# Kernel tuning notes

Hardware: AMD Instinct MI355X
Metric: run time of the kernel (lower is better)

## Reference

```python
import jax, jax.numpy as jnp
import numpy as np

D = 512        # feat_dim
H_ENC = 8      # motion_encoder heads
H_SA = 4       # semantic-aware attention heads
BS, L, N = 8, 512, 4096
LN_EPS = 1e-5


def _layernorm(x, g, b):
    m = jnp.mean(x, axis=-1, keepdims=True)
    v = jnp.var(x, axis=-1, keepdims=True)
    return (x - m) * jax.lax.rsqrt(v + LN_EPS) * g + b


def _linear(x, w, b):
    # torch nn.Linear convention: w [out, in]
    return x @ w.T + b


def setup_inputs() -> dict:
    key = jax.random.key(0)
    ks = jax.random.split(key, 24)
    s = 0.02
    inp = {
        "motion": jax.random.normal(ks[0], (BS, L, D), jnp.float32),
        "scene_xyz": jax.random.normal(ks[1], (BS, N, 3), jnp.float32),
        "scene_feats": jax.random.normal(ks[2], (BS, N, D), jnp.float32),
        "spatial_prior": jax.random.normal(ks[3], (BS, L, N), jnp.float32),
        # motion_encoder (pre-norm MHA + pre-norm MLP, both residual)
        "enc_ln1_g": jnp.ones((D,), jnp.float32),
        "enc_ln1_b": jnp.zeros((D,), jnp.float32),
        "enc_qkv_w": jax.random.normal(ks[4], (3 * D, D), jnp.float32) * s,
        "enc_qkv_b": jnp.zeros((3 * D,), jnp.float32),
        "enc_out_w": jax.random.normal(ks[5], (D, D), jnp.float32) * s,
        "enc_out_b": jnp.zeros((D,), jnp.float32),
        "enc_ln2_g": jnp.ones((D,), jnp.float32),
        "enc_ln2_b": jnp.zeros((D,), jnp.float32),
        "enc_ff1_w": jax.random.normal(ks[6], (D, D), jnp.float32) * s,
        "enc_ff1_b": jnp.zeros((D,), jnp.float32),
        "enc_ff2_w": jax.random.normal(ks[7], (D, D), jnp.float32) * s,
        "enc_ff2_b": jnp.zeros((D,), jnp.float32),
        # SemanticAwareAttention
        "sa_q_w": jax.random.normal(ks[8], (D, D), jnp.float32) * s,
        "sa_q_b": jnp.zeros((D,), jnp.float32),
        "sa_kv_w": jax.random.normal(ks[9], (2 * D, D), jnp.float32) * s,
        "sa_kv_b": jnp.zeros((2 * D,), jnp.float32),
        "sa_out_w": jax.random.normal(ks[10], (D, D), jnp.float32) * s,
        "sa_out_b": jnp.zeros((D,), jnp.float32),
        # final concat-MLP: in 2D -> 4D -> D  (Mlp(2D, D, expansion=4))
        "mlp_fc1_w": jax.random.normal(ks[11], (4 * D, 2 * D), jnp.float32) * s,
        "mlp_fc1_b": jnp.zeros((4 * D,), jnp.float32),
        "mlp_fc2_w": jax.random.normal(ks[12], (D, 4 * D), jnp.float32) * s,
        "mlp_fc2_b": jnp.zeros((D,), jnp.float32),
    }
    return inp


def _forward(motion, scene_xyz, scene_feats, spatial_prior,
             enc_ln1_g, enc_ln1_b, enc_qkv_w, enc_qkv_b, enc_out_w, enc_out_b,
             enc_ln2_g, enc_ln2_b, enc_ff1_w, enc_ff1_b, enc_ff2_w, enc_ff2_b,
             sa_q_w, sa_q_b, sa_kv_w, sa_kv_b, sa_out_w, sa_out_b,
             mlp_fc1_w, mlp_fc1_b, mlp_fc2_w, mlp_fc2_b):
    bs, slen, _ = motion.shape
    n = scene_feats.shape[1]
    dh_enc = D // H_ENC
    dh_sa = D // H_SA

    # ---- motion encoder: pre-norm MHA + residual ----
    h = _layernorm(motion, enc_ln1_g, enc_ln1_b)
    qkv = _linear(h, enc_qkv_w, enc_qkv_b)                      # [bs, L, 3D]
    q, k, v = jnp.split(qkv, 3, axis=-1)
    q = q.reshape(bs, slen, H_ENC, dh_enc)
    k = k.reshape(bs, slen, H_ENC, dh_enc)
    v = v.reshape(bs, slen, H_ENC, dh_enc)
    att = jnp.einsum("bqhd,bkhd->bhqk", q, k) * (dh_enc ** -0.5)
    att = jax.nn.softmax(att, axis=-1)
    o = jnp.einsum("bhqk,bkhd->bqhd", att, v).reshape(bs, slen, D)
    x = motion + _linear(o, enc_out_w, enc_out_b)

    # ---- pre-norm MLP + residual ----
    h2 = _layernorm(x, enc_ln2_g, enc_ln2_b)
    ff = _linear(jax.nn.gelu(_linear(h2, enc_ff1_w, enc_ff1_b), approximate=False),
                 enc_ff2_w, enc_ff2_b)
    motion_sca = x + ff

    # ---- SemanticAwareAttention ----
    q = _linear(motion_sca, sa_q_w, sa_q_b) * (D ** -0.5)       # scale by feat_dim (faithful)
    kv = _linear(scene_feats, sa_kv_w, sa_kv_b)
    k, v = jnp.split(kv, 2, axis=-1)
    # faithful to torch: q.view(bs, H, L, d) splits heads from flattened (L, D)
    q = q.reshape(bs, H_SA, slen, dh_sa)
    k = k.reshape(bs, n, H_SA, dh_sa).transpose(0, 2, 1, 3)     # [bs, H, N, d]
    v = v.reshape(bs, n, H_SA, dh_sa).transpose(0, 2, 1, 3)
    att = jnp.einsum("bhqd,bhkd->bhqk", q, k) + spatial_prior[:, None, :, :]
    att = jax.nn.softmax(att, axis=-1)
    sm = jnp.einsum("bhqk,bhkd->bqhd", att, v).reshape(bs, slen, D)
    sm_feature = _linear(sm, sa_out_w, sa_out_b)

    # ---- concat + MLP ----
    cat = jnp.concatenate([motion_sca, sm_feature], axis=-1)    # [bs, L, 2D]
    out = _linear(jax.nn.gelu(_linear(cat, mlp_fc1_w, mlp_fc1_b), approximate=False),
                  mlp_fc2_w, mlp_fc2_b)
    return out


def reference(motion, scene_xyz, scene_feats, spatial_prior,
              enc_ln1_g, enc_ln1_b, enc_qkv_w, enc_qkv_b, enc_out_w, enc_out_b,
              enc_ln2_g, enc_ln2_b, enc_ff1_w, enc_ff1_b, enc_ff2_w, enc_ff2_b,
              sa_q_w, sa_q_b, sa_kv_w, sa_kv_b, sa_out_w, sa_out_b,
              mlp_fc1_w, mlp_fc1_b, mlp_fc2_w, mlp_fc2_b):
    return _forward(motion, scene_xyz, scene_feats, spatial_prior,
                    enc_ln1_g, enc_ln1_b, enc_qkv_w, enc_qkv_b, enc_out_w, enc_out_b,
                    enc_ln2_g, enc_ln2_b, enc_ff1_w, enc_ff1_b, enc_ff2_w, enc_ff2_b,
                    sa_q_w, sa_q_b, sa_kv_w, sa_kv_b, sa_out_w, sa_out_b,
                    mlp_fc1_w, mlp_fc1_b, mlp_fc2_w, mlp_fc2_b)
```

## Files before the change

kernel.cpp:

```cpp
#include <hip/hip_runtime.h>

typedef unsigned short bf16_t;
typedef __attribute__((ext_vector_type(8))) short bf16x8;
typedef __attribute__((ext_vector_type(4))) float f32x4;

__device__ __forceinline__ float bf2f(bf16_t u) {
  union { unsigned int i; float f; } v; v.i = ((unsigned int)u) << 16; return v.f;
}
__device__ __forceinline__ bf16_t f2bf(float f) {
  union { float f; unsigned int i; } v; v.f = f;
  unsigned int u = v.i;
  u += 0x7fffu + ((u >> 16) & 1u);
  return (bf16_t)(u >> 16);
}
__device__ __forceinline__ float gelu_exact(float x) {
  return 0.5f * x * (1.0f + erff(x * 0.7071067811865475f));
}

__global__ __launch_bounds__(256) void f2bf_kernel(const float4* __restrict__ s,
                                                   ushort4* __restrict__ d, int n4) {
  int i = blockIdx.x * 256 + threadIdx.x;
  if (i < n4) {
    float4 f = s[i];
    ushort4 u; u.x = f2bf(f.x); u.y = f2bf(f.y); u.z = f2bf(f.z); u.w = f2bf(f.w);
    d[i] = u;
  }
}

__global__ __launch_bounds__(256) void ln_kernel(const float* __restrict__ x,
                                                 const float* __restrict__ g,
                                                 const float* __restrict__ bta,
                                                 bf16_t* __restrict__ y) {
  const int w = threadIdx.x >> 6, lane = threadIdx.x & 63;
  const long row = (long)blockIdx.x * 4 + w;
  const long base = row * 512;
  const int c0 = lane << 2;
  float v[8];
  float4 f0 = *(const float4*)(x + base + c0);
  float4 f1 = *(const float4*)(x + base + 256 + c0);
  v[0]=f0.x; v[1]=f0.y; v[2]=f0.z; v[3]=f0.w;
  v[4]=f1.x; v[5]=f1.y; v[6]=f1.z; v[7]=f1.w;
  float s = 0.f;
#pragma unroll
  for (int c=0;c<8;++c) s += v[c];
#pragma unroll
  for (int o=32;o>0;o>>=1) s += __shfl_xor(s, o);
  const float mean = s * 0.001953125f;
  float ss = 0.f;
#pragma unroll
  for (int c=0;c<8;++c) { float d = v[c]-mean; ss += d*d; }
#pragma unroll
  for (int o=32;o>0;o>>=1) ss += __shfl_xor(ss, o);
  const float rstd = rsqrtf(ss * 0.001953125f + 1e-5f);
  ushort4 o0, o1;
  o0.x = f2bf((v[0]-mean)*rstd*g[c0+0] + bta[c0+0]);
  o0.y = f2bf((v[1]-mean)*rstd*g[c0+1] + bta[c0+1]);
  o0.z = f2bf((v[2]-mean)*rstd*g[c0+2] + bta[c0+2]);
  o0.w = f2bf((v[3]-mean)*rstd*g[c0+3] + bta[c0+3]);
  o1.x = f2bf((v[4]-mean)*rstd*g[256+c0+0] + bta[256+c0+0]);
  o1.y = f2bf((v[5]-mean)*rstd*g[256+c0+1] + bta[256+c0+1]);
  o1.z = f2bf((v[6]-mean)*rstd*g[256+c0+2] + bta[256+c0+2]);
  o1.w = f2bf((v[7]-mean)*rstd*g[256+c0+3] + bta[256+c0+3]);
  *(ushort4*)(y + base + c0) = o0;
  *(ushort4*)(y + base + 256 + c0) = o1;
}

struct MmaNT {
  const bf16_t* A; const bf16_t* W; const float* bias; const float* res; void* C;
  long lda, sAb, sAh;
  long ldw, sWb, sWh;
  long ldr, sRb, sRh;
  long ldc, sCb, sCh;
  int K, zdiv, cBf, act;
  float scale;
};

template <int MT>
__global__ __launch_bounds__(256) void mma_nt_kernel(MmaNT p) {
  constexpr int FM = MT / 32;
  __shared__ __align__(16) bf16_t smem[MT * 128];
  const int tid = threadIdx.x;
  const int wid = tid >> 6, lane = tid & 63;
  const int wm = wid & 1, wn = wid >> 1;
  const int quad = lane >> 4, l16 = lane & 15;
  const int z = blockIdx.z;
  const int zb = z / p.zdiv, zh = z % p.zdiv;

  const int nbx = gridDim.x;
  const int nwg = nbx * gridDim.y;
  const int flat = blockIdx.y * nbx + blockIdx.x;
  const int sw = (flat & 7) * (nwg >> 3) + (flat >> 3);
  const int bx = sw % nbx, by = sw / nbx;

  const long m0 = (long)by * MT;
  const long n0 = (long)bx * 128;
  const bf16_t* Ag = p.A + (long)zb * p.sAb + (long)zh * p.sAh +
                     (m0 + wm * (MT / 2) + l16) * p.lda;
  const bf16_t* Wg = p.W + (long)zb * p.sWb + (long)zh * p.sWh +
                     (n0 + wn * 64 + l16) * p.ldw;

  f32x4 zero4 = {0.f, 0.f, 0.f, 0.f};
  f32x4 acc[FM][4];
#pragma unroll
  for (int fm = 0; fm < FM; ++fm)
#pragma unroll
    for (int fn = 0; fn < 4; ++fn) acc[fm][fn] = zero4;

  bf16x8 af[FM], wf[4];
#pragma unroll
  for (int fm = 0; fm < FM; ++fm)
    af[fm] = *(const bf16x8*)(Ag + (long)(fm * 16) * p.lda + quad * 8);
#pragma unroll
  for (int fn = 0; fn < 4; ++fn)
    wf[fn] = *(const bf16x8*)(Wg + (long)(fn * 16) * p.ldw + quad * 8);

  for (int kc = 0; kc < p.K; kc += 32) {
    bf16x8 afn[FM], wfn[4];
    const int kn = kc + 32;
    if (kn < p.K) {
#pragma unroll
      for (int fm = 0; fm < FM; ++fm)
        afn[fm] = *(const bf16x8*)(Ag + (long)(fm * 16) * p.lda + kn + quad * 8);
#pragma unroll
      for (int fn = 0; fn < 4; ++fn)
        wfn[fn] = *(const bf16x8*)(Wg + (long)(fn * 16) * p.ldw + kn + quad * 8);
    }
#pragma unroll
    for (int fm = 0; fm < FM; ++fm)
#pragma unroll
      for (int fn = 0; fn < 4; ++fn)
        acc[fm][fn] = __builtin_amdgcn_mfma_f32_16x16x32_bf16(af[fm], wf[fn], acc[fm][fn], 0, 0, 0);
#pragma unroll
    for (int fm = 0; fm < FM; ++fm) af[fm] = afn[fm];
#pragma unroll
    for (int fn = 0; fn < 4; ++fn) wf[fn] = wfn[fn];
  }

  const long cOff = (long)zb * p.sCb + (long)zh * p.sCh;
  const long rOff = (long)zb * p.sRb + (long)zh * p.sRh;
  if (p.cBf) {
#pragma unroll
    for (int fm = 0; fm < FM; ++fm) {
#pragma unroll
      for (int fn = 0; fn < 4; ++fn) {
        const int lc = wn * 64 + fn * 16 + l16;
        const long col = n0 + lc;
        const float bv = p.bias ? p.bias[col] : 0.f;
#pragma unroll
        for (int r = 0; r < 4; ++r) {
          const int lr = wm * (MT / 2) + fm * 16 + quad * 4 + r;
          float t = acc[fm][fn][r] + bv;
          if (p.act) t = gelu_exact(t);
          t *= p.scale;
          if (p.res) t += p.res[rOff + (m0 + lr) * p.ldr + col];
          smem[lr * 128 + lc] = f2bf(t);
        }
      }
    }
    __syncthreads();
    bf16_t* Cg = (bf16_t*)p.C + cOff + m0 * p.ldc + n0;
#pragma unroll
    for (int i = 0; i < MT / 16; ++i) {
      const int flat2 = tid + i * 256;
      const int r = flat2 >> 4, c = (flat2 & 15) * 8;
      *(uint4*)(Cg + (long)r * p.ldc + c) = *(const uint4*)&smem[r * 128 + c];
    }
  } else {
#pragma unroll
    for (int fm = 0; fm < FM; ++fm) {
#pragma unroll
      for (int fn = 0; fn < 4; ++fn) {
        const long col = n0 + wn * 64 + fn * 16 + l16;
        const float bv = p.bias ? p.bias[col] : 0.f;
#pragma unroll
        for (int r = 0; r < 4; ++r) {
          const long row = m0 + wm * (MT / 2) + fm * 16 + quad * 4 + r;
          float t = acc[fm][fn][r] + bv;
          if (p.act) t = gelu_exact(t);
          t *= p.scale;
          if (p.res) t += p.res[rOff + row * p.ldr + col];
          ((float*)p.C)[cOff + row * p.ldc + col] = t;
        }
      }
    }
  }
}

struct TransP {
  const bf16_t* src; bf16_t* dst;
  long sSb, sSh, ld;
  int nh, N, D;
};

__global__ __launch_bounds__(256) void transpose_kernel(TransP p) {
  __shared__ bf16_t T[64][72];
  const int tid = threadIdx.x;
  const int z = blockIdx.z;
  const int zb = z / p.nh, zh = z % p.nh;
  const long n0 = (long)blockIdx.x * 64;
  const long d0 = (long)blockIdx.y * 64;
  const bf16_t* src = p.src + (long)zb * p.sSb + (long)zh * p.sSh;
  bf16_t* dst = p.dst + (long)z * p.D * p.N;
#pragma unroll
  for (int i = 0; i < 2; ++i) {
    int flat = tid + i * 256, r = flat >> 3, cg = flat & 7;
    uint4 v = *(const uint4*)(src + (n0 + r) * p.ld + d0 + cg * 8);
    *(uint4*)&T[r][cg * 8] = v;
  }
  __syncthreads();
#pragma unroll
  for (int i = 0; i < 2; ++i) {
    int flat = tid + i * 256, dr = flat >> 3, ncg = flat & 7;
    uint4 o;
    unsigned int* op = (unsigned int*)&o;
#pragma unroll
    for (int j = 0; j < 4; ++j)
      op[j] = (unsigned int)T[ncg * 8 + 2 * j][dr] | ((unsigned int)T[ncg * 8 + 2 * j + 1][dr] << 16);
    *(uint4*)(dst + (d0 + dr) * p.N + n0 + ncg * 8) = o;
  }
}

struct FlashP2 {
  const bf16_t* Q; const bf16_t* K; const bf16_t* VT; const float* prior;
  float* partO; float* partML;
  long ldq, sQb, sQh;
  long ldk, sKb, sKh;
  long sVz, sPb;
  int nh, N, segN;
  float scale;
};

template <int DH, int HASP>
__global__ __launch_bounds__(256) void flash3_kernel(FlashP2 p) {
  constexpr int KK = DH / 32;
  constexpr int NFO = DH / 16;
  constexpr int KPAD = DH + 8;
  __shared__ bf16_t smem[64 * KPAD + DH * 72];
  bf16_t* Kl = smem;
  bf16_t* Pl = smem;
  bf16_t* Vl = smem + 64 * KPAD;
  const int tid = threadIdx.x;
  const int w = tid >> 6, lane = tid & 63;
  const int quad = lane >> 4, l16 = lane & 15;
  const int z = blockIdx.z;
  const int zb = z / p.nh, zh = z % p.nh;
  const int qr0 = blockIdx.y * 64 + w * 16;
  const bf16_t* Q = p.Q + (long)zb * p.sQb + (long)zh * p.sQh + (long)qr0 * p.ldq;
  const bf16_t* K = p.K + (long)zb * p.sKb + (long)zh * p.sKh;
  const bf16_t* VT = p.VT + (long)z * p.sVz;

  bf16x8 qf[KK];
#pragma unroll
  for (int kk = 0; kk < KK; ++kk)
    qf[kk] = *(const bf16x8*)(Q + (long)l16 * p.ldq + kk * 32 + quad * 8);

  f32x4 zero4 = {0.f, 0.f, 0.f, 0.f};
  f32x4 O[NFO];
  float m_[4], l_[4];
#pragma unroll
  for (int f = 0; f < NFO; ++f) O[f] = zero4;
#pragma unroll
  for (int r = 0; r < 4; ++r) { m_[r] = -1e30f; l_[r] = 0.f; }

  const int k0 = blockIdx.x * p.segN;
  for (int kt = k0; kt < k0 + p.segN; kt += 64) {
    __syncthreads();
    constexpr int KTH = DH / 8;
#pragma unroll
    for (int i = 0; i < DH / 32; ++i) {
      int flat = tid + i * 256, r = flat / KTH, c = (flat % KTH) * 8;
      *(uint4*)&Kl[r * KPAD + c] = *(const uint4*)(K + (long)(kt + r) * p.ldk + c);
    }
#pragma unroll
    for (int i = 0; i < DH / 32; ++i) {
      int flat = tid + i * 256, r = flat >> 3, c = (flat & 7) * 8;
      *(uint4*)&Vl[r * 72 + c] = *(const uint4*)(VT + (long)r * p.N + kt + c);
    }
    float pr[4][4];
    if (HASP) {
      const float* PR = p.prior + (long)zb * p.sPb +
                        (long)(qr0 + quad * 4) * p.N + kt;
#pragma unroll
      for (int nf = 0; nf < 4; ++nf)
#pragma unroll
        for (int r = 0; r < 4; ++r)
          pr[nf][r] = PR[(long)r * p.N + nf * 16 + l16];
    }
    __syncthreads();
    f32x4 s[4];
#pragma unroll
    for (int nf = 0; nf < 4; ++nf) s[nf] = zero4;
#pragma unroll
    for (int nf = 0; nf < 4; ++nf)
#pragma unroll
      for (int kk = 0; kk < KK; ++kk) {
        bf16x8 kf = *(const bf16x8*)&Kl[(nf * 16 + l16) * KPAD + kk * 32 + quad * 8];
        s[nf] = __builtin_amdgcn_mfma_f32_16x16x32_bf16(qf[kk], kf, s[nf], 0, 0, 0);
      }
    float tm[4];
#pragma unroll
    for (int r = 0; r < 4; ++r) tm[r] = -1e30f;
#pragma unroll
    for (int nf = 0; nf < 4; ++nf)
#pragma unroll
      for (int r = 0; r < 4; ++r) {
        float t = s[nf][r] * p.scale;
        if (HASP) t += pr[nf][r];
        s[nf][r] = t;
        tm[r] = fmaxf(tm[r], t);
      }
#pragma unroll
    for (int off = 1; off < 16; off <<= 1)
#pragma unroll
      for (int r = 0; r < 4; ++r) tm[r] = fmaxf(tm[r], __shfl_xor(tm[r], off));
    float alpha[4], rs[4];
#pragma unroll
    for (int r = 0; r < 4; ++r) {
      float mn = fmaxf(m_[r], tm[r]);
      alpha[r] = __expf(m_[r] - mn);
      m_[r] = mn;
      rs[r] = 0.f;
    }
#pragma unroll
    for (int nf = 0; nf < 4; ++nf)
#pragma unroll
      for (int r = 0; r < 4; ++r) {
        float pv = __expf(s[nf][r] - m_[r]);
        s[nf][r] = pv;
        rs[r] += pv;
      }
#pragma unroll
    for (int off = 1; off < 16; off <<= 1)
#pragma unroll
      for (int r = 0; r < 4; ++r) rs[r] += __shfl_xor(rs[r], off);
#pragma unroll
    for (int r = 0; r < 4; ++r) l_[r] = l_[r] * alpha[r] + rs[r];
    __syncthreads();
#pragma unroll
    for (int nf = 0; nf < 4; ++nf)
#pragma unroll
      for (int r = 0; r < 4; ++r)
        Pl[(w * 16 + quad * 4 + r) * 72 + nf * 16 + l16] = f2bf(s[nf][r]);
#pragma unroll
    for (int f = 0; f < NFO; ++f)
#pragma unroll
      for (int r = 0; r < 4; ++r) O[f][r] *= alpha[r];
    bf16x8 pf[2];
#pragma unroll
    for (int kk2 = 0; kk2 < 2; ++kk2)
      pf[kk2] = *(const bf16x8*)&Pl[(w * 16 + l16) * 72 + kk2 * 32 + quad * 8];
#pragma unroll
    for (int f = 0; f < NFO; ++f)
#pragma unroll
      for (int kk2 = 0; kk2 < 2; ++kk2) {
        bf16x8 vf = *(const bf16x8*)&Vl[(f * 16 + l16) * 72 + kk2 * 32 + quad * 8];
        O[f] = __builtin_amdgcn_mfma_f32_16x16x32_bf16(pf[kk2], vf, O[f], 0, 0, 0);
      }
  }
  const long t = ((long)z * gridDim.y + blockIdx.y) * gridDim.x + blockIdx.x;
  float* PO = p.partO + t * (64 * DH);
  float* PM = p.partML + t * 128;
  const int row = w * 16 + quad * 4;
#pragma unroll
  for (int f = 0; f < NFO; ++f)
#pragma unroll
    for (int r = 0; r < 4; ++r)
      PO[(long)(row + r) * DH + f * 16 + l16] = O[f][r];
  if (l16 == 0) {
#pragma unroll
    for (int r = 0; r < 4; ++r) {
      PM[(row + r) * 2 + 0] = m_[r];
      PM[(row + r) * 2 + 1] = l_[r];
    }
  }
}

struct MergeP {
  const float* partO; const float* partML; bf16_t* C;
  long ldc, sCb;
  int nh, y;
};

template <int DH, int NS>
__global__ __launch_bounds__(256) void fmerge_kernel(MergeP p) {
  const int tid = threadIdx.x;
  const int r = tid >> 2, ch = tid & 3;
  const int blk = blockIdx.x;
  const int z = blk / p.y, qb = blk % p.y;
  const int zb = z / p.nh, zh = z % p.nh;
  const long t0 = (long)blk * NS;
  float mm[NS], wgt[NS];
  float mstar = -1e30f;
#pragma unroll
  for (int s = 0; s < NS; ++s) {
    mm[s] = p.partML[(t0 + s) * 128 + r * 2];
    mstar = fmaxf(mstar, mm[s]);
  }
  float lsum = 0.f;
#pragma unroll
  for (int s = 0; s < NS; ++s) {
    wgt[s] = __expf(mm[s] - mstar);
    lsum += wgt[s] * p.partML[(t0 + s) * 128 + r * 2 + 1];
  }
  const float inv = 1.0f / lsum;
  const int c0 = ch * (DH / 4);
  bf16_t* Cp = p.C + (long)zb * p.sCb + (long)(qb * 64 + r) * p.ldc + (long)zh * DH + c0;
#pragma unroll
  for (int c = 0; c < DH / 4; c += 4) {
    float4 acc = make_float4(0.f, 0.f, 0.f, 0.f);
#pragma unroll
    for (int s = 0; s < NS; ++s) {
      float4 v = *(const float4*)(p.partO + (t0 + s) * (64 * DH) + (long)r * DH + c0 + c);
      acc.x += wgt[s] * v.x; acc.y += wgt[s] * v.y;
      acc.z += wgt[s] * v.z; acc.w += wgt[s] * v.w;
    }
    ushort4 o;
    o.x = f2bf(acc.x * inv); o.y = f2bf(acc.y * inv);
    o.z = f2bf(acc.z * inv); o.w = f2bf(acc.w * inv);
    *(ushort4*)(Cp + c) = o;
  }
}

#define MB(x) ((long)(x) << 20)

extern "C" void kernel_launch(void* const* d_in, const int* in_sizes, int n_in,
                              void* d_out, int out_size, void* d_ws, size_t ws_size,
                              hipStream_t stream) {
  const float* motion      = (const float*)d_in[0];
  const float* scene_feats = (const float*)d_in[2];
  const float* prior       = (const float*)d_in[3];
  const float* ln1_g = (const float*)d_in[4];
  const float* ln1_b = (const float*)d_in[5];
  const float* qkv_w = (const float*)d_in[6];
  const float* qkv_b = (const float*)d_in[7];
  const float* out_w = (const float*)d_in[8];
  const float* out_b = (const float*)d_in[9];
  const float* ln2_g = (const float*)d_in[10];
  const float* ln2_b = (const float*)d_in[11];
  const float* ff1_w = (const float*)d_in[12];
  const float* ff1_b = (const float*)d_in[13];
  const float* ff2_w = (const float*)d_in[14];
  const float* ff2_b = (const float*)d_in[15];
  const float* saq_w = (const float*)d_in[16];
  const float* saq_b = (const float*)d_in[17];
  const float* sakv_w = (const float*)d_in[18];
  const float* sakv_b = (const float*)d_in[19];
  const float* saout_w = (const float*)d_in[20];
  const float* saout_b = (const float*)d_in[21];
  const float* fc1_w = (const float*)d_in[22];
  const float* fc1_b = (const float*)d_in[23];
  const float* fc2_w = (const float*)d_in[24];
  const float* fc2_b = (const float*)d_in[25];

  char* W = (char*)d_ws;
  bf16_t* h_bf    = (bf16_t*)(W + MB(0));
  float*  x_f     = (float*) (W + MB(4));
  bf16_t* o_ff    = (bf16_t*)(W + MB(12));
  bf16_t* qkv_bf  = (bf16_t*)(W + MB(16));
  bf16_t* qsa     = (bf16_t*)(W + MB(28));
  bf16_t* sm_bf   = (bf16_t*)(W + MB(32));
  bf16_t* cat_bf  = (bf16_t*)(W + MB(36));
  bf16_t* fc1g    = (bf16_t*)(W + MB(44));
  bf16_t* vTe     = (bf16_t*)(W + MB(60));
  bf16_t* kv_bf   = (bf16_t*)(W + MB(64));
  bf16_t* vT      = (bf16_t*)(W + MB(128));
  bf16_t* wbase   = (bf16_t*)(W + MB(160));
  bf16_t* scene_bf= (bf16_t*)(W + MB(172));

  float* encO  = (float*)fc1g;
  float* encML = (float*)cat_bf;
  float* saO   = (float*)scene_bf;
  float* saML  = (float*)vTe;

  bf16_t* wq   = wbase + 0L;
  bf16_t* wout = wbase + 786432L;
  bf16_t* wff1 = wbase + 1048576L;
  bf16_t* wff2 = wbase + 1310720L;
  bf16_t* wsaq = wbase + 1572864L;
  bf16_t* wskv = wbase + 1835008L;
  bf16_t* wsout= wbase + 2359296L;
  bf16_t* wfc1 = wbase + 2621440L;
  bf16_t* wfc2 = wbase + 4718592L;

  const dim3 B256(256);
  auto cvt = [&](const float* s, bf16_t* d, long n) {
    int n4 = (int)(n / 4);
    f2bf_kernel<<<(n4 + 255) / 256, B256, 0, stream>>>((const float4*)s, (ushort4*)d, n4);
  };
  cvt(qkv_w,  wq,   786432);
  cvt(out_w,  wout, 262144);
  cvt(ff1_w,  wff1, 262144);
  cvt(ff2_w,  wff2, 262144);
  cvt(saq_w,  wsaq, 262144);
  cvt(sakv_w, wskv, 524288);
  cvt(saout_w,wsout,262144);
  cvt(fc1_w,  wfc1, 2097152);
  cvt(fc2_w,  wfc2, 1048576);
  cvt(scene_feats, scene_bf, 16777216);

  ln_kernel<<<1024, B256, 0, stream>>>(motion, ln1_g, ln1_b, h_bf);

  { MmaNT p{}; p.scale=1.f; p.zdiv=1; p.cBf=1;
    p.A=h_bf; p.lda=512; p.W=wq; p.ldw=512; p.bias=qkv_b;
    p.C=qkv_bf; p.ldc=1536; p.K=512;
    mma_nt_kernel<128><<<dim3(12,32,1), B256, 0, stream>>>(p); }

  { TransP t{}; t.src=qkv_bf+1024; t.dst=vTe; t.sSb=786432; t.sSh=64;
    t.ld=1536; t.nh=8; t.N=512; t.D=64;
    transpose_kernel<<<dim3(8,1,64), B256, 0, stream>>>(t); }
  { FlashP2 p{};
    p.Q=qkv_bf;     p.ldq=1536; p.sQb=786432; p.sQh=64;
    p.K=qkv_bf+512; p.ldk=1536; p.sKb=786432; p.sKh=64;
    p.VT=vTe; p.sVz=32768;
    p.prior=nullptr; p.sPb=0;
    p.partO=encO; p.partML=encML;
    p.nh=8; p.N=512; p.segN=256; p.scale=0.125f;
    flash3_kernel<64,0><<<dim3(2,8,64), B256, 0, stream>>>(p); }
  { MergeP m{}; m.partO=encO; m.partML=encML; m.C=o_ff;
    m.ldc=512; m.sCb=262144; m.nh=8; m.y=8;
    fmerge_kernel<64,2><<<512, B256, 0, stream>>>(m); }

  { MmaNT p{}; p.scale=1.f; p.zdiv=1;
    p.A=o_ff; p.lda=512; p.W=wout; p.ldw=512; p.bias=out_b;
    p.res=motion; p.ldr=512;
    p.C=x_f; p.ldc=512; p.K=512;
    mma_nt_kernel<64><<<dim3(4,64,1), B256, 0, stream>>>(p); }

  ln_kernel<<<1024, B256, 0, stream>>>(x_f, ln2_g, ln2_b, h_bf);

  { MmaNT p{}; p.scale=1.f; p.zdiv=1; p.cBf=1; p.act=1;
    p.A=h_bf; p.lda=512; p.W=wff1; p.ldw=512; p.bias=ff1_b;
    p.C=o_ff; p.ldc=512; p.K=512;
    mma_nt_kernel<64><<<dim3(4,64,1), B256, 0, stream>>>(p); }

  { MmaNT p{}; p.scale=1.f; p.zdiv=1; p.cBf=1;
    p.A=o_ff; p.lda=512; p.W=wff2; p.ldw=512; p.bias=ff2_b;
    p.res=x_f; p.ldr=512;
    p.C=cat_bf; p.ldc=1024; p.K=512;
    mma_nt_kernel<64><<<dim3(4,64,1), B256, 0, stream>>>(p); }

  { MmaNT p{}; p.zdiv=1; p.cBf=1; p.scale=0.04419417382415922f;
    p.A=cat_bf; p.lda=1024; p.W=wsaq; p.ldw=512; p.bias=saq_b;
    p.C=qsa; p.ldc=512; p.K=512;
    mma_nt_kernel<64><<<dim3(4,64,1), B256, 0, stream>>>(p); }

  { MmaNT p{}; p.scale=1.f; p.zdiv=1; p.cBf=1;
    p.A=scene_bf; p.lda=512; p.W=wskv; p.ldw=512; p.bias=sakv_b;
    p.C=kv_bf; p.ldc=1024; p.K=512;
    mma_nt_kernel<128><<<dim3(8,256,1), B256, 0, stream>>>(p); }

  { TransP t{}; t.src=kv_bf+512; t.dst=vT; t.sSb=4194304; t.sSh=128;
    t.ld=1024; t.nh=4; t.N=4096; t.D=128;
    transpose_kernel<<<dim3(64,2,32), B256, 0, stream>>>(t); }
  { FlashP2 p{};
    p.Q=qsa;   p.ldq=128;  p.sQb=262144;  p.sQh=65536;
    p.K=kv_bf; p.ldk=1024; p.sKb=4194304; p.sKh=128;
    p.VT=vT; p.sVz=524288;
    p.prior=prior; p.sPb=2097152;
    p.partO=saO; p.partML=saML;
    p.nh=4; p.N=4096; p.segN=1024; p.scale=1.f;
    flash3_kernel<128,1><<<dim3(4,8,32), B256, 0, stream>>>(p); }
  { MergeP m{}; m.partO=saO; m.partML=saML; m.C=sm_bf;
    m.ldc=512; m.sCb=262144; m.nh=4; m.y=8;
    fmerge_kernel<128,4><<<256, B256, 0, stream>>>(m); }

  { MmaNT p{}; p.scale=1.f; p.zdiv=1; p.cBf=1;
    p.A=sm_bf; p.lda=512; p.W=wsout; p.ldw=512; p.bias=saout_b;
    p.C=cat_bf + 512; p.ldc=1024; p.K=512;
    mma_nt_kernel<64><<<dim3(4,64,1), B256, 0, stream>>>(p); }

  { MmaNT p{}; p.scale=1.f; p.zdiv=1; p.cBf=1; p.act=1;
    p.A=cat_bf; p.lda=1024; p.W=wfc1; p.ldw=1024; p.bias=fc1_b;
    p.C=fc1g; p.ldc=2048; p.K=1024;
    mma_nt_kernel<128><<<dim3(16,32,1), B256, 0, stream>>>(p); }

  { MmaNT p{}; p.scale=1.f; p.zdiv=1;
    p.A=fc1g; p.lda=2048; p.W=wfc2; p.ldw=2048; p.bias=fc2_b;
    p.C=d_out; p.ldc=512; p.K=2048;
    mma_nt_kernel<64><<<dim3(4,64,1), B256, 0, stream>>>(p); }
}
```

Before: 796.9 us.

## Stage GEMM tiles in LDS via direct global-to-LDS loads for 128-row tiles

For the MT=128 GEMM variant, A and W k-slices are now loaded cooperatively into shared memory with global_load_lds, and each wave reads its MFMA fragments from LDS. Before, every wave loaded its fragments straight from global memory, so tiles shared across waves were fetched more than once. The new path is single-buffered and places two block barriers around each 32-wide k step, which drops the register prefetch overlap the old loop had. The smaller MT variant keeps the old direct-load path.

```diff
diff --git a/kernel.cpp b/kernel.cpp
--- a/kernel.cpp
+++ b/kernel.cpp
@@ -15,6 +15,11 @@
 }
 __device__ __forceinline__ float gelu_exact(float x) {
   return 0.5f * x * (1.0f + erff(x * 0.7071067811865475f));
+}
+__device__ __forceinline__ void g2l16(bf16_t* l, const bf16_t* g) {
+  __builtin_amdgcn_global_load_lds(
+      (const __attribute__((address_space(1))) unsigned int*)g,
+      (__attribute__((address_space(3))) unsigned int*)l, 16, 0, 0);
 }
 
 __global__ __launch_bounds__(256) void f2bf_kernel(const float4* __restrict__ s,
@@ -78,7 +83,12 @@
 template <int MT>
 __global__ __launch_bounds__(256) void mma_nt_kernel(MmaNT p) {
   constexpr int FM = MT / 32;
-  __shared__ __align__(16) bf16_t smem[MT * 128];
+  constexpr int TILE_E = (MT + 128) * 32;
+  constexpr int ST_E = MT * 128;
+  constexpr int SM_E = (TILE_E > ST_E) ? TILE_E : ST_E;
+  __shared__ __align__(16) bf16_t smem[SM_E];
+  bf16_t* Al = smem;
+  bf16_t* Wl = smem + MT * 32;
   const int tid = threadIdx.x;
   const int wid = tid >> 6, lane = tid & 63;
   const int wm = wid & 1, wn = wid >> 1;
@@ -94,10 +104,6 @@
 
   const long m0 = (long)by * MT;
   const long n0 = (long)bx * 128;
-  const bf16_t* Ag = p.A + (long)zb * p.sAb + (long)zh * p.sAh +
-                     (m0 + wm * (MT / 2) + l16) * p.lda;
-  const bf16_t* Wg = p.W + (long)zb * p.sWb + (long)zh * p.sWh +
-                     (n0 + wn * 64 + l16) * p.ldw;
 
   f32x4 zero4 = {0.f, 0.f, 0.f, 0.f};
   f32x4 acc[FM][4];
@@ -106,34 +112,68 @@
 #pragma unroll
     for (int fn = 0; fn < 4; ++fn) acc[fm][fn] = zero4;
 
-  bf16x8 af[FM], wf[4];
-#pragma unroll
-  for (int fm = 0; fm < FM; ++fm)
-    af[fm] = *(const bf16x8*)(Ag + (long)(fm * 16) * p.lda + quad * 8);
-#pragma unroll
-  for (int fn = 0; fn < 4; ++fn)
-    wf[fn] = *(const bf16x8*)(Wg + (long)(fn * 16) * p.ldw + quad * 8);
-
-  for (int kc = 0; kc < p.K; kc += 32) {
-    bf16x8 afn[FM], wfn[4];
-    const int kn = kc + 32;
-    if (kn < p.K) {
+  if constexpr (MT == 128) {
+    const bf16_t* Ag = p.A + (long)zb * p.sAb + (long)zh * p.sAh + m0 * p.lda;
+    const bf16_t* Wg = p.W + (long)zb * p.sWb + (long)zh * p.sWh + n0 * p.ldw;
+    const int sr = lane >> 2;
+    const int sc = (lane & 3) * 8;
+    for (int kc = 0; kc < p.K; kc += 32) {
+#pragma unroll
+      for (int j = 0; j < 2; ++j)
+        g2l16(&Al[(j * 64 + wid * 16) * 32],
+              Ag + (long)(j * 64 + wid * 16 + sr) * p.lda + kc + sc);
+#pragma unroll
+      for (int j = 0; j < 2; ++j)
+        g2l16(&Wl[(j * 64 + wid * 16) * 32],
+              Wg + (long)(j * 64 + wid * 16 + sr) * p.ldw + kc + sc);
+      __syncthreads();
+      bf16x8 af[FM], wf[4];
 #pragma unroll
       for (int fm = 0; fm < FM; ++fm)
-        afn[fm] = *(const bf16x8*)(Ag + (long)(fm * 16) * p.lda + kn + quad * 8);
+        af[fm] = *(const bf16x8*)&Al[(wm * 64 + fm * 16 + l16) * 32 + quad * 8];
 #pragma unroll
       for (int fn = 0; fn < 4; ++fn)
-        wfn[fn] = *(const bf16x8*)(Wg + (long)(fn * 16) * p.ldw + kn + quad * 8);
-    }
+        wf[fn] = *(const bf16x8*)&Wl[(wn * 64 + fn * 16 + l16) * 32 + quad * 8];
+#pragma unroll
+      for (int fm = 0; fm < FM; ++fm)
+#pragma unroll
+        for (int fn = 0; fn < 4; ++fn)
+          acc[fm][fn] = __builtin_amdgcn_mfma_f32_16x16x32_bf16(af[fm], wf[fn], acc[fm][fn], 0, 0, 0);
+      __syncthreads();
+    }
+  } else {
+    const bf16_t* Ag = p.A + (long)zb * p.sAb + (long)zh * p.sAh +
+                       (m0 + wm * (MT / 2) + l16) * p.lda;
+    const bf16_t* Wg = p.W + (long)zb * p.sWb + (long)zh * p.sWh +
+                       (n0 + wn * 64 + l16) * p.ldw;
+    bf16x8 af[FM], wf[4];
 #pragma unroll
     for (int fm = 0; fm < FM; ++fm)
-#pragma unroll
-      for (int fn = 0; fn < 4; ++fn)
-        acc[fm][fn] = __builtin_amdgcn_mfma_f32_16x16x32_bf16(af[fm], wf[fn], acc[fm][fn], 0, 0, 0);
-#pragma unroll
-    for (int fm = 0; fm < FM; ++fm) af[fm] = afn[fm];
-#pragma unroll
-    for (int fn = 0; fn < 4; ++fn) wf[fn] = wfn[fn];
+      af[fm] = *(const bf16x8*)(Ag + (long)(fm * 16) * p.lda + quad * 8);
+#pragma unroll
+    for (int fn = 0; fn < 4; ++fn)
+      wf[fn] = *(const bf16x8*)(Wg + (long)(fn * 16) * p.ldw + quad * 8);
+    for (int kc = 0; kc < p.K; kc += 32) {
+      bf16x8 afn[FM], wfn[4];
+      const int kn = kc + 32;
+      if (kn < p.K) {
+#pragma unroll
+        for (int fm = 0; fm < FM; ++fm)
+          afn[fm] = *(const bf16x8*)(Ag + (long)(fm * 16) * p.lda + kn + quad * 8);
+#pragma unroll
+        for (int fn = 0; fn < 4; ++fn)
+          wfn[fn] = *(const bf16x8*)(Wg + (long)(fn * 16) * p.ldw + kn + quad * 8);
+      }
+#pragma unroll
+      for (int fm = 0; fm < FM; ++fm)
+#pragma unroll
+        for (int fn = 0; fn < 4; ++fn)
+          acc[fm][fn] = __builtin_amdgcn_mfma_f32_16x16x32_bf16(af[fm], wf[fn], acc[fm][fn], 0, 0, 0);
+#pragma unroll
+      for (int fm = 0; fm < FM; ++fm) af[fm] = afn[fm];
+#pragma unroll
+      for (int fn = 0; fn < 4; ++fn) wf[fn] = wfn[fn];
+    }
   }
 
   const long cOff = (long)zb * p.sCb + (long)zh * p.sCh;
```

After: 700.0 us. 12.2% less time.
